# Kernel tuning notes

Hardware: AMD Instinct MI355X
Metric: run time of the kernel (lower is better)

The kernel has to match this reference:

```python
import jax, jax.numpy as jnp
import numpy as np

H = 64  # hidden dim
D_IN = 15  # per-step feature dim


def _gru_layer(x, Wih, Whh, bih, bhh):
    """torch-style GRU, batch_first. x: [M, T, D] -> [M, T, H]."""
    xp = x @ Wih.T + bih  # [M, T, 3H], precomputed input projections

    def step(h, xt):
        gh = h @ Whh.T + bhh
        xr, xz, xn = jnp.split(xt, 3, axis=-1)
        hr, hz, hn = jnp.split(gh, 3, axis=-1)
        r = jax.nn.sigmoid(xr + hr)
        z = jax.nn.sigmoid(xz + hz)
        n = jnp.tanh(xn + r * hn)
        h_new = (1.0 - z) * n + z * h
        return h_new, h_new

    h0 = jnp.zeros((x.shape[0], Whh.shape[1]), x.dtype)
    _, hs = jax.lax.scan(step, h0, jnp.swapaxes(xp, 0, 1))  # [T, M, H]
    return jnp.swapaxes(hs, 0, 1)


def setup_inputs() -> dict:
    key = jax.random.key(0)
    ks = jax.random.split(key, 16)
    N, B, T = 500, 32, 32
    s = 0.05
    return {
        "raw": jax.random.normal(ks[0], (N, B, T, D_IN), dtype=jnp.float32),
        # GRU layer 1 (input 15 -> 64)
        "gru1_Wih": jax.random.normal(ks[1], (3 * H, D_IN), dtype=jnp.float32) * s,
        "gru1_Whh": jax.random.normal(ks[2], (3 * H, H), dtype=jnp.float32) * s,
        "gru1_bih": jax.random.normal(ks[3], (3 * H,), dtype=jnp.float32) * s,
        "gru1_bhh": jax.random.normal(ks[4], (3 * H,), dtype=jnp.float32) * s,
        # GRU layer 2 (64 -> 64)
        "gru2_Wih": jax.random.normal(ks[5], (3 * H, H), dtype=jnp.float32) * s,
        "gru2_Whh": jax.random.normal(ks[6], (3 * H, H), dtype=jnp.float32) * s,
        "gru2_bih": jax.random.normal(ks[7], (3 * H,), dtype=jnp.float32) * s,
        "gru2_bhh": jax.random.normal(ks[8], (3 * H,), dtype=jnp.float32) * s,
        # temporal attention fc (64 -> 1)
        "attn_W": jax.random.normal(ks[9], (1, H), dtype=jnp.float32) * s,
        "attn_b": jax.random.normal(ks[10], (1,), dtype=jnp.float32) * s,
        # GAT attention-block linear W (64 -> 64) and u (128,)
        "gat_W_w": jax.random.normal(ks[11], (H, H), dtype=jnp.float32) * s,
        "gat_W_b": jax.random.normal(ks[12], (H,), dtype=jnp.float32) * s,
        "gat_u": jax.random.normal(ks[13], (2 * H,), dtype=jnp.float32) * s,
        # GAT value projection W1 (64 -> 64)
        "gat_W1_w": jax.random.normal(ks[14], (H, H), dtype=jnp.float32) * s,
        "gat_W1_b": jax.random.normal(ks[15], (H,), dtype=jnp.float32) * s,
    }


def reference(raw, gru1_Wih, gru1_Whh, gru1_bih, gru1_bhh,
              gru2_Wih, gru2_Whh, gru2_bih, gru2_bhh,
              attn_W, attn_b, gat_W_w, gat_W_b, gat_u, gat_W1_w, gat_W1_b):
    N, B, T, D = raw.shape
    x = raw.reshape(N * B, T, D)

    # SequenceEncoder: two stacked GRUs + temporal attention (dropout = eval identity)
    h = _gru_layer(x, gru1_Wih, gru1_Whh, gru1_bih, gru1_bhh)
    h = _gru_layer(h, gru2_Wih, gru2_Whh, gru2_bih, gru2_bhh)  # [NB, T, H]
    scores = jnp.tanh(h @ attn_W.T + attn_b)                    # [NB, T, 1]
    w = jax.nn.softmax(scores, axis=1)                          # softmax over time
    Ai = jnp.sum(h * w, axis=1).reshape(N, B, H)                # [N, B, H]

    # GAT over all-to-all node graph
    sq = Ai @ gat_W_w.T + gat_W_b          # attention-block projection [N, B, H]
    s_q = sq @ gat_u[:H]                   # query-side score [N, B]
    s_k = sq @ gat_u[H:]                   # neighbor-side score [N, B]
    score = s_q[:, None, :] + s_k[None, :, :]                   # [Nq, Nk, B]
    beta = jnp.exp(jax.nn.leaky_relu(score, negative_slope=0.01))
    beta = beta / jnp.sum(beta, axis=1, keepdims=True)          # normalize over neighbors
    proj = Ai @ gat_W1_w.T + gat_W1_b                           # value projection [N, B, H]
    g = jax.nn.relu(jnp.einsum('qkb,kbd->qbd', beta, proj))     # [N, B, H]
    return g
```

## Files before the change

kernel.cpp:

```cpp
#include <hip/hip_runtime.h>

#define TT 32
#define DIN 15
#define LOG2E 1.44269504088896340736f

typedef _Float16 f16x8 __attribute__((ext_vector_type(8)));
typedef _Float16 f16x4 __attribute__((ext_vector_type(4)));
typedef float f32x4 __attribute__((ext_vector_type(4)));

__device__ __forceinline__ float rcp_(float x){ return __builtin_amdgcn_rcpf(x); }
__device__ __forceinline__ float exp2_(float x){ return __builtin_amdgcn_exp2f(x); }
__device__ __forceinline__ float tanh_(float x){ return fmaf(-2.f, rcp_(__expf(2.f*x)+1.f), 1.f); }

#define MFMA(a,b,c) __builtin_amdgcn_mfma_f32_16x16x32_f16(a,b,c,0,0,0)

__device__ __forceinline__ f16x8 f16x8_zero(){
  f16x8 v;
  #pragma unroll
  for (int j=0;j<8;++j) v[j]=(_Float16)0.f;
  return v;
}

__global__ void wprep(const float* __restrict__ w1ih, const float* __restrict__ w1hh,
                      const float* __restrict__ w2ih, const float* __restrict__ w2hh,
                      const float* __restrict__ b1ih, const float* __restrict__ b1hh,
                      const float* __restrict__ W1,
                      const float* __restrict__ Ww, const float* __restrict__ Wb,
                      const float* __restrict__ u,
                      _Float16* __restrict__ wf, float* __restrict__ vqk){
  int id = blockIdx.x*256 + threadIdx.x;
  if (id < 47104){
    int e = id & 7, c = id >> 3;
    float v, scale;
    if (c < 4608){
      int mat = c / 1536; int r = c - mat*1536;
      int lane = r & 63, kf = (r>>6)&1, q = r>>7;
      const float* W = (mat==0)? w1hh : (mat==1)? w2ih : w2hh;
      int ht = q/3, g3 = q - ht*3;
      int row = g3*64 + ht*16 + (lane & 15);
      int k = kf*32 + (lane>>4)*8 + e;
      v = W[row*64 + k];
      scale = (g3==2) ? 2.f*LOG2E : -LOG2E;
    } else if (c < 5376){
      int r = c - 4608; int lane = r & 63, q = r>>6;
      int ht = q/3, g3 = q - ht*3;
      int row = g3*64 + ht*16 + (lane & 15);
      int k = (lane>>4)*8 + e;
      if (k < DIN)       v = w1ih[row*DIN + k];
      else if (k == DIN) v = (g3 < 2) ? (b1ih[row] + b1hh[row]) : b1ih[row];
      else               v = 0.f;
      scale = (g3==2) ? 2.f*LOG2E : -LOG2E;
    } else {
      int r = c - 5376; int lane = r & 63, q = r>>6;
      int ht = q>>1, kf = q&1;
      int row = ht*16 + (lane & 15);
      int k = kf*32 + (lane>>4)*8 + e;
      v = W1[row*64 + k]; scale = 1.f;
    }
    wf[c*8 + e] = (_Float16)(v*scale);
  } else if (id < 47104 + 130){
    int t = id - 47104;
    if (t < 128){
      int which = t>>6, j = t&63;
      float s = 0.f;
      for (int i=0;i<64;++i) s = fmaf(u[which*64+i], Ww[i*64+j], s);
      vqk[t] = s;
    } else {
      int which = t-128;
      float s = 0.f;
      for (int i=0;i<64;++i) s = fmaf(u[which*64+i], Wb[i], s);
      vqk[128+which] = s;
    }
  }
}

__global__ __launch_bounds__(256, 2) void gru_mfma(
    const float* __restrict__ raw,
    const _Float16* __restrict__ wf,
    const float* __restrict__ vqk,
    const float* __restrict__ bhh1,
    const float* __restrict__ bih2, const float* __restrict__ bhh2,
    const float* __restrict__ attnW, const float* __restrict__ attnb,
    const float* __restrict__ W1b,
    _Float16* __restrict__ projh, float* __restrict__ sqT, float* __restrict__ skT)
{
  __shared__ _Float16 xfh[TT*64*8];
  __shared__ _Float16 h1s[2][32*64];
  __shared__ _Float16 h2s[2][32*64];
  __shared__ float bias2[256];
  __shared__ float attp[2][2][4][16];
  __shared__ float attq[4][32], attk[4][32];

  const int tid  = threadIdx.x;
  const int lane = tid & 63;
  const int ht   = tid >> 6;
  const int g    = lane >> 4;
  const int sl   = lane & 15;
  const int s7   = sl & 7;
  const int n    = blockIdx.x;
  const int seq0 = n*32;
  const int row0 = ht*16 + g*4;

  { int* z2 = (int*)h2s[0]; for (int i=tid; i<1024; i+=256) z2[i]=0; }
  if (tid < 64){
    bias2[tid]       = -(bih2[tid]      + bhh2[tid])   *LOG2E;
    bias2[64+tid]    = -(bih2[64+tid]   + bhh2[64+tid])*LOG2E;
    bias2[128+tid]   =  bih2[128+tid]*(2.f*LOG2E);
    bias2[192+tid]   =  bhh2[128+tid]*(2.f*LOG2E);
  }
  for (int idx=tid; idx<TT*32; idx+=256){
    int s = idx & 31, t = idx >> 5;
    const float* rp = &raw[(size_t)(seq0+s)*(TT*DIN) + t*DIN];
    f16x8 lo, hi;
    #pragma unroll
    for (int j=0;j<8;++j){
      lo[j] = (_Float16)rp[j];
      hi[j] = (j<7) ? (_Float16)rp[8+j] : (_Float16)1.0f;
    }
    *(f16x8*)(xfh + ((size_t)t*64 +      s)*8) = lo;
    *(f16x8*)(xfh + ((size_t)t*64 + 32 + s)*8) = hi;
  }

  const f16x8* wf8 = (const f16x8*)wf;
  f16x8 wr1_0 = wf8[((ht*3+0)*2+0)*64 + lane], wr1_1 = wf8[((ht*3+0)*2+1)*64 + lane];
  f16x8 wz1_0 = wf8[((ht*3+1)*2+0)*64 + lane], wz1_1 = wf8[((ht*3+1)*2+1)*64 + lane];
  f16x8 wn1_0 = wf8[((ht*3+2)*2+0)*64 + lane], wn1_1 = wf8[((ht*3+2)*2+1)*64 + lane];
  f16x8 ar2_0 = wf8[1536+((ht*3+0)*2+0)*64 + lane], ar2_1 = wf8[1536+((ht*3+0)*2+1)*64 + lane];
  f16x8 az2_0 = wf8[1536+((ht*3+1)*2+0)*64 + lane], az2_1 = wf8[1536+((ht*3+1)*2+1)*64 + lane];
  f16x8 an2_0 = wf8[1536+((ht*3+2)*2+0)*64 + lane], an2_1 = wf8[1536+((ht*3+2)*2+1)*64 + lane];
  f16x8 br2_0 = wf8[3072+((ht*3+0)*2+0)*64 + lane], br2_1 = wf8[3072+((ht*3+0)*2+1)*64 + lane];
  f16x8 bz2_0 = wf8[3072+((ht*3+1)*2+0)*64 + lane], bz2_1 = wf8[3072+((ht*3+1)*2+1)*64 + lane];
  f16x8 bn2_0 = wf8[3072+((ht*3+2)*2+0)*64 + lane], bn2_1 = wf8[3072+((ht*3+2)*2+1)*64 + lane];
  f16x8 xr1 = wf8[4608 + (ht*3+0)*64 + lane];
  f16x8 xz1 = wf8[4608 + (ht*3+1)*64 + lane];
  f16x8 xn1 = wf8[4608 + (ht*3+2)*64 + lane];

  f32x4 Bhn1, awv;
  #pragma unroll
  for (int r=0;r<4;++r){ Bhn1[r] = bhh1[128+row0+r]*(2.f*LOG2E); awv[r] = attnW[row0+r]; }
  const float ab = attnb[0];

  __syncthreads();

  const f16x8 fz = f16x8_zero();
  f32x4 h1c0={0,0,0,0}, h1c1={0,0,0,0}, h2c0={0,0,0,0}, h2c1={0,0,0,0};
  f32x4 num0={0,0,0,0}, num1={0,0,0,0};
  float den0=0.f, den1=0.f;
  const int cwr = (((ht*2+(g>>1)) ^ s7))*8 + (g&1)*4;

  {
    f16x8 xf0 = fz, xf1 = fz;
    if (g < 2){
      xf0 = *(const f16x8*)(xfh + ((size_t)0*64 + g*32 +      sl)*8);
      xf1 = *(const f16x8*)(xfh + ((size_t)0*64 + g*32 + 16 + sl)*8);
    }
    f32x4 Cr0={0,0,0,0}, Cz0={0,0,0,0}, Cxn0={0,0,0,0}, Chn0=Bhn1;
    f32x4 Cr1={0,0,0,0}, Cz1={0,0,0,0}, Cxn1={0,0,0,0}, Chn1=Bhn1;
    Cr0 = MFMA(xr1,xf0,Cr0); Cz0 = MFMA(xz1,xf0,Cz0); Cxn0 = MFMA(xn1,xf0,Cxn0);
    Cr1 = MFMA(xr1,xf1,Cr1); Cz1 = MFMA(xz1,xf1,Cz1); Cxn1 = MFMA(xn1,xf1,Cxn1);
    f16x4 hw0, hw1;
    #pragma unroll
    for (int r=0;r<4;++r){
      float rg0 = rcp_(1.f + exp2_(Cr0[r]));
      float zg0 = rcp_(1.f + exp2_(Cz0[r]));
      float ng0 = fmaf(-2.f, rcp_(exp2_(Cxn0[r] + rg0*Chn0[r]) + 1.f), 1.f);
      float h0  = ng0 - zg0*ng0;
      h1c0[r] = h0; hw0[r] = (_Float16)h0;
      float rg1 = rcp_(1.f + exp2_(Cr1[r]));
      float zg1 = rcp_(1.f + exp2_(Cz1[r]));
      float ng1 = fmaf(-2.f, rcp_(exp2_(Cxn1[r] + rg1*Chn1[r]) + 1.f), 1.f);
      float h1v = ng1 - zg1*ng1;
      h1c1[r] = h1v; hw1[r] = (_Float16)h1v;
    }
    *(f16x4*)(h1s[0] + sl*64      + cwr) = hw0;
    *(f16x4*)(h1s[0] + (16+sl)*64 + cwr) = hw1;
  }
  __syncthreads();

  #pragma unroll 1
  for (int i=0; i<TT; ++i){
    const _Float16* h1rd = h1s[i&1];
    const _Float16* h2rd = h2s[i&1];
    _Float16* h1wr = h1s[(i+1)&1];
    _Float16* h2wr = h2s[(i+1)&1];
    f16x8 h1f0_0 = *(const f16x8*)(h1rd + sl*64      + ((g    ^s7))*8);
    f16x8 h1f0_1 = *(const f16x8*)(h1rd + sl*64      + (((4+g)^s7))*8);
    f16x8 h1f1_0 = *(const f16x8*)(h1rd + (16+sl)*64 + ((g    ^s7))*8);
    f16x8 h1f1_1 = *(const f16x8*)(h1rd + (16+sl)*64 + (((4+g)^s7))*8);
    f16x8 h2f0_0 = *(const f16x8*)(h2rd + sl*64      + ((g    ^s7))*8);
    f16x8 h2f0_1 = *(const f16x8*)(h2rd + sl*64      + (((4+g)^s7))*8);
    f16x8 h2f1_0 = *(const f16x8*)(h2rd + (16+sl)*64 + ((g    ^s7))*8);
    f16x8 h2f1_1 = *(const f16x8*)(h2rd + (16+sl)*64 + (((4+g)^s7))*8);
    const int tn = (i < TT-1) ? i+1 : TT-1;
    f16x8 xf0 = fz, xf1 = fz;
    if (g < 2){
      xf0 = *(const f16x8*)(xfh + ((size_t)tn*64 + g*32 +      sl)*8);
      xf1 = *(const f16x8*)(xfh + ((size_t)tn*64 + g*32 + 16 + sl)*8);
    }
    if (i > 0){
      const float (*ap)[4][16] = attp[(i+1)&1];
      float s40 = ap[0][0][sl]+ap[0][1][sl]+ap[0][2][sl]+ap[0][3][sl];
      float s41 = ap[1][0][sl]+ap[1][1][sl]+ap[1][2][sl]+ap[1][3][sl];
      float e0 = __expf(tanh_(s40 + ab));
      float e1 = __expf(tanh_(s41 + ab));
      den0 += e0; den1 += e1;
      #pragma unroll
      for (int r=0;r<4;++r){
        num0[r] = fmaf(e0, h2c0[r], num0[r]);
        num1[r] = fmaf(e1, h2c1[r], num1[r]);
      }
    }
    f32x4 Dr0  = *(const f32x4*)(bias2 + row0);
    f32x4 Dz0  = *(const f32x4*)(bias2 + 64 + row0);
    f32x4 Dxn0 = *(const f32x4*)(bias2 + 128 + row0);
    f32x4 Dhn0 = *(const f32x4*)(bias2 + 192 + row0);
    f32x4 Dr1 = Dr0, Dz1 = Dz0, Dxn1 = Dxn0, Dhn1 = Dhn0;
    Dr0  = MFMA(ar2_0,h1f0_0,Dr0);  Dr0  = MFMA(ar2_1,h1f0_1,Dr0);
    Dr0  = MFMA(br2_0,h2f0_0,Dr0);  Dr0  = MFMA(br2_1,h2f0_1,Dr0);
    Dr1  = MFMA(ar2_0,h1f1_0,Dr1);  Dr1  = MFMA(ar2_1,h1f1_1,Dr1);
    Dr1  = MFMA(br2_0,h2f1_0,Dr1);  Dr1  = MFMA(br2_1,h2f1_1,Dr1);
    Dz0  = MFMA(az2_0,h1f0_0,Dz0);  Dz0  = MFMA(az2_1,h1f0_1,Dz0);
    Dz0  = MFMA(bz2_0,h2f0_0,Dz0);  Dz0  = MFMA(bz2_1,h2f0_1,Dz0);
    Dz1  = MFMA(az2_0,h1f1_0,Dz1);  Dz1  = MFMA(az2_1,h1f1_1,Dz1);
    Dz1  = MFMA(bz2_0,h2f1_0,Dz1);  Dz1  = MFMA(bz2_1,h2f1_1,Dz1);
    Dxn0 = MFMA(an2_0,h1f0_0,Dxn0); Dxn0 = MFMA(an2_1,h1f0_1,Dxn0);
    Dxn1 = MFMA(an2_0,h1f1_0,Dxn1); Dxn1 = MFMA(an2_1,h1f1_1,Dxn1);
    Dhn0 = MFMA(bn2_0,h2f0_0,Dhn0); Dhn0 = MFMA(bn2_1,h2f0_1,Dhn0);
    Dhn1 = MFMA(bn2_0,h2f1_0,Dhn1); Dhn1 = MFMA(bn2_1,h2f1_1,Dhn1);
    f32x4 Cr0={0,0,0,0}, Cz0={0,0,0,0}, Cxn0={0,0,0,0}, Chn0=Bhn1;
    f32x4 Cr1={0,0,0,0}, Cz1={0,0,0,0}, Cxn1={0,0,0,0}, Chn1=Bhn1;
    Cr0 = MFMA(wr1_0,h1f0_0,Cr0); Cr0 = MFMA(wr1_1,h1f0_1,Cr0); Cr0 = MFMA(xr1,xf0,Cr0);
    Cr1 = MFMA(wr1_0,h1f1_0,Cr1); Cr1 = MFMA(wr1_1,h1f1_1,Cr1); Cr1 = MFMA(xr1,xf1,Cr1);
    Cz0 = MFMA(wz1_0,h1f0_0,Cz0); Cz0 = MFMA(wz1_1,h1f0_1,Cz0); Cz0 = MFMA(xz1,xf0,Cz0);
    Cz1 = MFMA(wz1_0,h1f1_0,Cz1); Cz1 = MFMA(wz1_1,h1f1_1,Cz1); Cz1 = MFMA(xz1,xf1,Cz1);
    Chn0 = MFMA(wn1_0,h1f0_0,Chn0); Chn0 = MFMA(wn1_1,h1f0_1,Chn0);
    Chn1 = MFMA(wn1_0,h1f1_0,Chn1); Chn1 = MFMA(wn1_1,h1f1_1,Chn1);
    Cxn0 = MFMA(xn1,xf0,Cxn0);
    Cxn1 = MFMA(xn1,xf1,Cxn1);
    f16x4 hw0, hw1;
    float p0 = 0.f, p1 = 0.f;
    #pragma unroll
    for (int r=0;r<4;++r){
      float rg0 = rcp_(1.f + exp2_(Dr0[r]));
      float zg0 = rcp_(1.f + exp2_(Dz0[r]));
      float ng0 = fmaf(-2.f, rcp_(exp2_(Dxn0[r] + rg0*Dhn0[r]) + 1.f), 1.f);
      float h0  = ng0 + zg0*(h2c0[r] - ng0);
      h2c0[r] = h0; hw0[r] = (_Float16)h0;
      p0 = fmaf(h0, awv[r], p0);
      float rg1 = rcp_(1.f + exp2_(Dr1[r]));
      float zg1 = rcp_(1.f + exp2_(Dz1[r]));
      float ng1 = fmaf(-2.f, rcp_(exp2_(Dxn1[r] + rg1*Dhn1[r]) + 1.f), 1.f);
      float h1v = ng1 + zg1*(h2c1[r] - ng1);
      h2c1[r] = h1v; hw1[r] = (_Float16)h1v;
      p1 = fmaf(h1v, awv[r], p1);
    }
    *(f16x4*)(h2wr + sl*64      + cwr) = hw0;
    *(f16x4*)(h2wr + (16+sl)*64 + cwr) = hw1;
    p0 += __shfl_xor(p0, 16, 64); p0 += __shfl_xor(p0, 32, 64);
    p1 += __shfl_xor(p1, 16, 64); p1 += __shfl_xor(p1, 32, 64);
    if (lane < 16){ attp[i&1][0][ht][sl] = p0; attp[i&1][1][ht][sl] = p1; }
    if (i < TT-1){
      #pragma unroll
      for (int r=0;r<4;++r){
        float rg0 = rcp_(1.f + exp2_(Cr0[r]));
        float zg0 = rcp_(1.f + exp2_(Cz0[r]));
        float ng0 = fmaf(-2.f, rcp_(exp2_(Cxn0[r] + rg0*Chn0[r]) + 1.f), 1.f);
        float h0  = ng0 + zg0*(h1c0[r] - ng0);
        h1c0[r] = h0; hw0[r] = (_Float16)h0;
        float rg1 = rcp_(1.f + exp2_(Cr1[r]));
        float zg1 = rcp_(1.f + exp2_(Cz1[r]));
        float ng1 = fmaf(-2.f, rcp_(exp2_(Cxn1[r] + rg1*Chn1[r]) + 1.f), 1.f);
        float h1v = ng1 + zg1*(h1c1[r] - ng1);
        h1c1[r] = h1v; hw1[r] = (_Float16)h1v;
      }
      *(f16x4*)(h1wr + sl*64      + cwr) = hw0;
      *(f16x4*)(h1wr + (16+sl)*64 + cwr) = hw1;
    }
    __syncthreads();
  }
  {
    const float (*ap)[4][16] = attp[1];
    float s40 = ap[0][0][sl]+ap[0][1][sl]+ap[0][2][sl]+ap[0][3][sl];
    float s41 = ap[1][0][sl]+ap[1][1][sl]+ap[1][2][sl]+ap[1][3][sl];
    float e0 = __expf(tanh_(s40 + ab));
    float e1 = __expf(tanh_(s41 + ab));
    den0 += e0; den1 += e1;
    #pragma unroll
    for (int r=0;r<4;++r){
      num0[r] = fmaf(e0, h2c0[r], num0[r]);
      num1[r] = fmaf(e1, h2c1[r], num1[r]);
    }
  }
  float rd0 = rcp_(den0), rd1 = rcp_(den1);
  f32x4 av0, av1;
  #pragma unroll
  for (int r=0;r<4;++r){ av0[r] = num0[r]*rd0; av1[r] = num1[r]*rd1; }
  {
    f32x4 vq4 = *(const f32x4*)&vqk[row0];
    f32x4 vk4 = *(const f32x4*)&vqk[64+row0];
    float pq0=0.f, pk0=0.f, pq1=0.f, pk1=0.f;
    #pragma unroll
    for (int r=0;r<4;++r){
      pq0 = fmaf(av0[r], vq4[r], pq0); pk0 = fmaf(av0[r], vk4[r], pk0);
      pq1 = fmaf(av1[r], vq4[r], pq1); pk1 = fmaf(av1[r], vk4[r], pk1);
    }
    pq0 += __shfl_xor(pq0,16,64); pq0 += __shfl_xor(pq0,32,64);
    pk0 += __shfl_xor(pk0,16,64); pk0 += __shfl_xor(pk0,32,64);
    pq1 += __shfl_xor(pq1,16,64); pq1 += __shfl_xor(pq1,32,64);
    pk1 += __shfl_xor(pk1,16,64); pk1 += __shfl_xor(pk1,32,64);
    if (lane < 16){
      attq[ht][sl] = pq0;    attk[ht][sl] = pk0;
      attq[ht][16+sl] = pq1; attk[ht][16+sl] = pk1;
    }
  }
  { f16x4 af0, af1;
    #pragma unroll
    for (int r=0;r<4;++r){ af0[r] = (_Float16)av0[r]; af1[r] = (_Float16)av1[r]; }
    *(f16x4*)(h1s[0] + sl*64      + cwr) = af0;
    *(f16x4*)(h1s[0] + (16+sl)*64 + cwr) = af1; }
  __syncthreads();
  if (tid < 32){
    float q4 = attq[0][tid]+attq[1][tid]+attq[2][tid]+attq[3][tid];
    float k4 = attk[0][tid]+attk[1][tid]+attk[2][tid]+attk[3][tid];
    sqT[tid*512 + n] = (q4 + vqk[128])*LOG2E;
    skT[tid*512 + n] = (k4 + vqk[129])*LOG2E;
  }
  {
    f16x8 a0 = wf8[5376 + (ht*2+0)*64 + lane];
    f16x8 a1 = wf8[5376 + (ht*2+1)*64 + lane];
    f16x8 b00 = *(const f16x8*)(h1s[0] + sl*64      + ((g    ^s7))*8);
    f16x8 b01 = *(const f16x8*)(h1s[0] + sl*64      + (((4+g)^s7))*8);
    f16x8 b10 = *(const f16x8*)(h1s[0] + (16+sl)*64 + ((g    ^s7))*8);
    f16x8 b11 = *(const f16x8*)(h1s[0] + (16+sl)*64 + (((4+g)^s7))*8);
    f32x4 P0 = *(const f32x4*)&W1b[row0];
    f32x4 P1 = P0;
    P0 = MFMA(a0,b00,P0); P0 = MFMA(a1,b01,P0);
    P1 = MFMA(a0,b10,P1); P1 = MFMA(a1,b11,P1);
    f16x4 pf0, pf1;
    #pragma unroll
    for (int r=0;r<4;++r){ pf0[r] = (_Float16)P0[r]; pf1[r] = (_Float16)P1[r]; }
    *(f16x4*)(projh + (size_t)(seq0+sl)*64    + row0) = pf0;
    *(f16x4*)(projh + (size_t)(seq0+16+sl)*64 + row0) = pf1;
  }
}

__global__ __launch_bounds__(256) void gat_agg(
    const _Float16* __restrict__ projh,
    const float* __restrict__ sqT, const float* __restrict__ skT,
    float* __restrict__ out)
{
  __shared__ _Float16 pT[64*64];
  __shared__ float sks[512];
  const int tid  = threadIdx.x;
  const int lane = tid & 63;
  const int wv   = tid >> 6;
  const int b    = blockIdx.x & 31;
  const int qt   = blockIdx.x >> 5;
  const int sl   = lane & 15, g = lane >> 4;
  const int myq  = qt*64 + wv*16 + sl;
  const float sq_l = (myq < 500) ? sqT[b*512 + myq] : -1e30f;
  for (int j = tid; j < 512; j += 256) sks[j] = (j < 500) ? skT[b*512 + j] : -1e30f;

  f32x4 acc[4] = {{0,0,0,0},{0,0,0,0},{0,0,0,0},{0,0,0,0}};
  float den_l = 0.f;
  const int kr = tid & 63, dgrp = tid >> 6;

  f16x8 pv0 = f16x8_zero(), pv1 = f16x8_zero();
  if (kr < 500){
    const f16x8* pp = (const f16x8*)(projh + ((size_t)kr*32 + b)*64 + dgrp*16);
    pv0 = pp[0]; pv1 = pp[1];
  }

  #pragma unroll 1
  for (int kc=0; kc<8; ++kc){
    __syncthreads();
    { char* base = (char*)pT;
      const int klo = (kr & 7) << 1, khi = kr >> 3;
      #pragma unroll
      for (int j=0;j<16;++j){
        int d = dgrp*16 + j;
        _Float16 v = (j<8) ? pv0[j] : pv1[j-8];
        *(_Float16*)(base + d*128 + (((khi ^ (d&7))) << 4) + klo) = v;
      } }
    __syncthreads();
    if (kc < 7){
      int node = (kc+1)*64 + kr;
      if (node < 500){
        const f16x8* pp = (const f16x8*)(projh + ((size_t)node*32 + b)*64 + dgrp*16);
        pv0 = pp[0]; pv1 = pp[1];
      } else { pv0 = f16x8_zero(); pv1 = f16x8_zero(); }
    }
    #pragma unroll
    for (int kc32=0; kc32<2; ++kc32){
      const int kb = kc*64 + kc32*32 + g*8;
      float4 skv0 = *(const float4*)&sks[kb];
      float4 skv1 = *(const float4*)&sks[kb+4];
      float s[8] = {sq_l+skv0.x, sq_l+skv0.y, sq_l+skv0.z, sq_l+skv0.w,
                    sq_l+skv1.x, sq_l+skv1.y, sq_l+skv1.z, sq_l+skv1.w};
      f16x8 bf;
      #pragma unroll
      for (int e=0;e<8;++e){
        float sc = fmaxf(s[e], 0.01f*s[e]);
        float ev = exp2_(sc);
        den_l += ev;
        bf[e] = (_Float16)ev;
      }
      const char* base = (const char*)pT;
      #pragma unroll
      for (int dt=0; dt<4; ++dt){
        f16x8 a = *(const f16x8*)(base + (dt*16 + sl)*128 + (((kc32*4 + g) ^ (sl&7)) << 4));
        acc[dt] = MFMA(a, bf, acc[dt]);
      }
    }
  }
  den_l += __shfl_xor(den_l, 16, 64);
  den_l += __shfl_xor(den_l, 32, 64);
  const float rd = rcp_(den_l);
  if (myq < 500){
    #pragma unroll
    for (int dt=0; dt<4; ++dt){
      f32x4 o;
      #pragma unroll
      for (int r=0;r<4;++r) o[r] = fmaxf(acc[dt][r]*rd, 0.f);
      *(f32x4*)&out[((size_t)myq*32 + b)*64 + dt*16 + g*4] = o;
    }
  }
}

extern "C" void kernel_launch(void* const* d_in, const int* in_sizes, int n_in,
                              void* d_out, int out_size, void* d_ws, size_t ws_size,
                              hipStream_t stream) {
  const float* raw   = (const float*)d_in[0];
  const float* w1ih  = (const float*)d_in[1];
  const float* w1hh  = (const float*)d_in[2];
  const float* b1ih  = (const float*)d_in[3];
  const float* b1hh  = (const float*)d_in[4];
  const float* w2ih  = (const float*)d_in[5];
  const float* w2hh  = (const float*)d_in[6];
  const float* b2ih  = (const float*)d_in[7];
  const float* b2hh  = (const float*)d_in[8];
  const float* attW  = (const float*)d_in[9];
  const float* attb  = (const float*)d_in[10];
  const float* gWw   = (const float*)d_in[11];
  const float* gWb   = (const float*)d_in[12];
  const float* gu    = (const float*)d_in[13];
  const float* gW1   = (const float*)d_in[14];
  const float* gW1b  = (const float*)d_in[15];
  float* outp = (float*)d_out;

  char* wsb = (char*)d_ws;
  _Float16* projh = (_Float16*)wsb;
  float*    sqT   = (float*)(wsb + 2048000);
  float*    skT   = (float*)(wsb + 2048000 + 65536);
  _Float16* wfh   = (_Float16*)(wsb + 2048000 + 131072);
  float*    vqk   = (float*)(wsb + 2048000 + 131072 + 94208);

  wprep<<<185, 256, 0, stream>>>(w1ih, w1hh, w2ih, w2hh, b1ih, b1hh,
                                 gW1, gWw, gWb, gu, wfh, vqk);
  gru_mfma<<<500, 256, 0, stream>>>(raw, wfh, vqk, b1hh, b2ih, b2hh,
                                    attW, attb, gW1b, projh, sqT, skT);
  gat_agg<<<256, 256, 0, stream>>>(projh, sqT, skT, outp);
}
```

Before: 92.24 us.

## Split GRU layers across warp roles in a 512-thread block

The block doubles to 512 threads. Waves 0-3 run the layer-1 GRU recurrence and waves 4-7 run layer-2 plus the temporal attention, so the two layers advance in a wavefront within each time step. Each wave now keeps only one layer's weights in registers. The aim is to halve the serial MFMA and transcendental chain per wave per step and to relieve register pressure. In exchange it adds more waves per block that must synchronise at every step, and the layer-2 state is reread from LDS as fp16 rather than kept in fp32 registers.

```diff
diff --git a/kernel.cpp b/kernel.cpp
--- a/kernel.cpp
+++ b/kernel.cpp
@@ -74,7 +74,7 @@
   }
 }
 
-__global__ __launch_bounds__(256, 2) void gru_mfma(
+__global__ __launch_bounds__(512, 4) void gru_mfma(
     const float* __restrict__ raw,
     const _Float16* __restrict__ wf,
     const float* __restrict__ vqk,
@@ -93,22 +93,27 @@
 
   const int tid  = threadIdx.x;
   const int lane = tid & 63;
-  const int ht   = tid >> 6;
+  const int wid  = tid >> 6;
+  const int role = wid >> 2;
+  const int ht   = wid & 3;
   const int g    = lane >> 4;
   const int sl   = lane & 15;
   const int s7   = sl & 7;
   const int n    = blockIdx.x;
   const int seq0 = n*32;
   const int row0 = ht*16 + g*4;
-
-  { int* z2 = (int*)h2s[0]; for (int i=tid; i<1024; i+=256) z2[i]=0; }
+  const int cwr  = (((ht*2+(g>>1)) ^ s7))*8 + (g&1)*4;
+  const int oT0  = sl*64, oT1 = (16+sl)*64;
+  const int c0   = (g ^ s7)*8, c1 = ((4+g) ^ s7)*8;
+
+  { int* z2 = (int*)h2s[0]; for (int i=tid; i<1024; i+=512) z2[i]=0; }
   if (tid < 64){
     bias2[tid]       = -(bih2[tid]      + bhh2[tid])   *LOG2E;
     bias2[64+tid]    = -(bih2[64+tid]   + bhh2[64+tid])*LOG2E;
     bias2[128+tid]   =  bih2[128+tid]*(2.f*LOG2E);
     bias2[192+tid]   =  bhh2[128+tid]*(2.f*LOG2E);
   }
-  for (int idx=tid; idx<TT*32; idx+=256){
+  for (int idx=tid; idx<TT*32; idx+=512){
     int s = idx & 31, t = idx >> 5;
     const float* rp = &raw[(size_t)(seq0+s)*(TT*DIN) + t*DIN];
     f16x8 lo, hi;
@@ -122,180 +127,195 @@
   }
 
   const f16x8* wf8 = (const f16x8*)wf;
-  f16x8 wr1_0 = wf8[((ht*3+0)*2+0)*64 + lane], wr1_1 = wf8[((ht*3+0)*2+1)*64 + lane];
-  f16x8 wz1_0 = wf8[((ht*3+1)*2+0)*64 + lane], wz1_1 = wf8[((ht*3+1)*2+1)*64 + lane];
-  f16x8 wn1_0 = wf8[((ht*3+2)*2+0)*64 + lane], wn1_1 = wf8[((ht*3+2)*2+1)*64 + lane];
-  f16x8 ar2_0 = wf8[1536+((ht*3+0)*2+0)*64 + lane], ar2_1 = wf8[1536+((ht*3+0)*2+1)*64 + lane];
-  f16x8 az2_0 = wf8[1536+((ht*3+1)*2+0)*64 + lane], az2_1 = wf8[1536+((ht*3+1)*2+1)*64 + lane];
-  f16x8 an2_0 = wf8[1536+((ht*3+2)*2+0)*64 + lane], an2_1 = wf8[1536+((ht*3+2)*2+1)*64 + lane];
-  f16x8 br2_0 = wf8[3072+((ht*3+0)*2+0)*64 + lane], br2_1 = wf8[3072+((ht*3+0)*2+1)*64 + lane];
-  f16x8 bz2_0 = wf8[3072+((ht*3+1)*2+0)*64 + lane], bz2_1 = wf8[3072+((ht*3+1)*2+1)*64 + lane];
-  f16x8 bn2_0 = wf8[3072+((ht*3+2)*2+0)*64 + lane], bn2_1 = wf8[3072+((ht*3+2)*2+1)*64 + lane];
-  f16x8 xr1 = wf8[4608 + (ht*3+0)*64 + lane];
-  f16x8 xz1 = wf8[4608 + (ht*3+1)*64 + lane];
-  f16x8 xn1 = wf8[4608 + (ht*3+2)*64 + lane];
-
-  f32x4 Bhn1, awv;
-  #pragma unroll
-  for (int r=0;r<4;++r){ Bhn1[r] = bhh1[128+row0+r]*(2.f*LOG2E); awv[r] = attnW[row0+r]; }
+  const f16x8 fz = f16x8_zero();
+  f16x8 A0,A1,A2,A3,A4,A5,A6,A7,A8,A9,A10,A11;
+  f32x4 BC;
   const float ab = attnb[0];
+  if (role == 0){
+    A0 = wf8[((ht*3+0)*2+0)*64 + lane]; A1 = wf8[((ht*3+0)*2+1)*64 + lane];
+    A2 = wf8[((ht*3+1)*2+0)*64 + lane]; A3 = wf8[((ht*3+1)*2+1)*64 + lane];
+    A4 = wf8[((ht*3+2)*2+0)*64 + lane]; A5 = wf8[((ht*3+2)*2+1)*64 + lane];
+    A6 = wf8[4608 + (ht*3+0)*64 + lane];
+    A7 = wf8[4608 + (ht*3+1)*64 + lane];
+    A8 = wf8[4608 + (ht*3+2)*64 + lane];
+    A9  = wf8[5376 + (ht*2+0)*64 + lane];
+    A10 = wf8[5376 + (ht*2+1)*64 + lane];
+    A11 = fz;
+    #pragma unroll
+    for (int r=0;r<4;++r) BC[r] = bhh1[128+row0+r]*(2.f*LOG2E);
+  } else {
+    A0 = wf8[1536+((ht*3+0)*2+0)*64+lane]; A1 = wf8[1536+((ht*3+0)*2+1)*64+lane];
+    A2 = wf8[1536+((ht*3+1)*2+0)*64+lane]; A3 = wf8[1536+((ht*3+1)*2+1)*64+lane];
+    A4 = wf8[1536+((ht*3+2)*2+0)*64+lane]; A5 = wf8[1536+((ht*3+2)*2+1)*64+lane];
+    A6 = wf8[3072+((ht*3+0)*2+0)*64+lane]; A7 = wf8[3072+((ht*3+0)*2+1)*64+lane];
+    A8 = wf8[3072+((ht*3+1)*2+0)*64+lane]; A9 = wf8[3072+((ht*3+1)*2+1)*64+lane];
+    A10= wf8[3072+((ht*3+2)*2+0)*64+lane]; A11= wf8[3072+((ht*3+2)*2+1)*64+lane];
+    #pragma unroll
+    for (int r=0;r<4;++r) BC[r] = attnW[row0+r];
+  }
+
+  f32x4 S0 = {0,0,0,0}, S1 = {0,0,0,0};
+  float d0 = 0.f, d1 = 0.f;
 
   __syncthreads();
 
-  const f16x8 fz = f16x8_zero();
-  f32x4 h1c0={0,0,0,0}, h1c1={0,0,0,0}, h2c0={0,0,0,0}, h2c1={0,0,0,0};
-  f32x4 num0={0,0,0,0}, num1={0,0,0,0};
-  float den0=0.f, den1=0.f;
-  const int cwr = (((ht*2+(g>>1)) ^ s7))*8 + (g&1)*4;
-
-  {
+  if (role == 0){
     f16x8 xf0 = fz, xf1 = fz;
     if (g < 2){
       xf0 = *(const f16x8*)(xfh + ((size_t)0*64 + g*32 +      sl)*8);
       xf1 = *(const f16x8*)(xfh + ((size_t)0*64 + g*32 + 16 + sl)*8);
     }
-    f32x4 Cr0={0,0,0,0}, Cz0={0,0,0,0}, Cxn0={0,0,0,0}, Chn0=Bhn1;
-    f32x4 Cr1={0,0,0,0}, Cz1={0,0,0,0}, Cxn1={0,0,0,0}, Chn1=Bhn1;
-    Cr0 = MFMA(xr1,xf0,Cr0); Cz0 = MFMA(xz1,xf0,Cz0); Cxn0 = MFMA(xn1,xf0,Cxn0);
-    Cr1 = MFMA(xr1,xf1,Cr1); Cz1 = MFMA(xz1,xf1,Cz1); Cxn1 = MFMA(xn1,xf1,Cxn1);
+    f32x4 Cr0={0,0,0,0}, Cz0={0,0,0,0}, Cxn0={0,0,0,0};
+    f32x4 Cr1={0,0,0,0}, Cz1={0,0,0,0}, Cxn1={0,0,0,0};
+    Cr0 = MFMA(A6,xf0,Cr0); Cz0 = MFMA(A7,xf0,Cz0); Cxn0 = MFMA(A8,xf0,Cxn0);
+    Cr1 = MFMA(A6,xf1,Cr1); Cz1 = MFMA(A7,xf1,Cz1); Cxn1 = MFMA(A8,xf1,Cxn1);
     f16x4 hw0, hw1;
     #pragma unroll
     for (int r=0;r<4;++r){
       float rg0 = rcp_(1.f + exp2_(Cr0[r]));
       float zg0 = rcp_(1.f + exp2_(Cz0[r]));
-      float ng0 = fmaf(-2.f, rcp_(exp2_(Cxn0[r] + rg0*Chn0[r]) + 1.f), 1.f);
+      float ng0 = fmaf(-2.f, rcp_(exp2_(Cxn0[r] + rg0*BC[r]) + 1.f), 1.f);
       float h0  = ng0 - zg0*ng0;
-      h1c0[r] = h0; hw0[r] = (_Float16)h0;
+      S0[r] = h0; hw0[r] = (_Float16)h0;
       float rg1 = rcp_(1.f + exp2_(Cr1[r]));
       float zg1 = rcp_(1.f + exp2_(Cz1[r]));
-      float ng1 = fmaf(-2.f, rcp_(exp2_(Cxn1[r] + rg1*Chn1[r]) + 1.f), 1.f);
+      float ng1 = fmaf(-2.f, rcp_(exp2_(Cxn1[r] + rg1*BC[r]) + 1.f), 1.f);
       float h1v = ng1 - zg1*ng1;
-      h1c1[r] = h1v; hw1[r] = (_Float16)h1v;
-    }
-    *(f16x4*)(h1s[0] + sl*64      + cwr) = hw0;
-    *(f16x4*)(h1s[0] + (16+sl)*64 + cwr) = hw1;
+      S1[r] = h1v; hw1[r] = (_Float16)h1v;
+    }
+    *(f16x4*)(h1s[0] + oT0 + cwr) = hw0;
+    *(f16x4*)(h1s[0] + oT1 + cwr) = hw1;
   }
   __syncthreads();
 
   #pragma unroll 1
   for (int i=0; i<TT; ++i){
-    const _Float16* h1rd = h1s[i&1];
-    const _Float16* h2rd = h2s[i&1];
-    _Float16* h1wr = h1s[(i+1)&1];
-    _Float16* h2wr = h2s[(i+1)&1];
-    f16x8 h1f0_0 = *(const f16x8*)(h1rd + sl*64      + ((g    ^s7))*8);
-    f16x8 h1f0_1 = *(const f16x8*)(h1rd + sl*64      + (((4+g)^s7))*8);
-    f16x8 h1f1_0 = *(const f16x8*)(h1rd + (16+sl)*64 + ((g    ^s7))*8);
-    f16x8 h1f1_1 = *(const f16x8*)(h1rd + (16+sl)*64 + (((4+g)^s7))*8);
-    f16x8 h2f0_0 = *(const f16x8*)(h2rd + sl*64      + ((g    ^s7))*8);
-    f16x8 h2f0_1 = *(const f16x8*)(h2rd + sl*64      + (((4+g)^s7))*8);
-    f16x8 h2f1_0 = *(const f16x8*)(h2rd + (16+sl)*64 + ((g    ^s7))*8);
-    f16x8 h2f1_1 = *(const f16x8*)(h2rd + (16+sl)*64 + (((4+g)^s7))*8);
-    const int tn = (i < TT-1) ? i+1 : TT-1;
-    f16x8 xf0 = fz, xf1 = fz;
-    if (g < 2){
-      xf0 = *(const f16x8*)(xfh + ((size_t)tn*64 + g*32 +      sl)*8);
-      xf1 = *(const f16x8*)(xfh + ((size_t)tn*64 + g*32 + 16 + sl)*8);
-    }
-    if (i > 0){
-      const float (*ap)[4][16] = attp[(i+1)&1];
+    if (role == 0){
+      if (i < TT-1){
+        const _Float16* h1rd = h1s[i&1];
+        _Float16* h1wr = h1s[(i+1)&1];
+        f16x8 xf0 = fz, xf1 = fz;
+        if (g < 2){
+          xf0 = *(const f16x8*)(xfh + ((size_t)(i+1)*64 + g*32 +      sl)*8);
+          xf1 = *(const f16x8*)(xfh + ((size_t)(i+1)*64 + g*32 + 16 + sl)*8);
+        }
+        f32x4 Cr0={0,0,0,0}, Cz0={0,0,0,0}, Cxn0={0,0,0,0}, Chn0=BC;
+        f32x4 Cr1={0,0,0,0}, Cz1={0,0,0,0}, Cxn1={0,0,0,0}, Chn1=BC;
+        f16x8 f0 = *(const f16x8*)(h1rd + oT0 + c0);
+        f16x8 f1 = *(const f16x8*)(h1rd + oT1 + c0);
+        Cr0 = MFMA(A0,f0,Cr0); Cz0 = MFMA(A2,f0,Cz0); Chn0 = MFMA(A4,f0,Chn0);
+        Cr1 = MFMA(A0,f1,Cr1); Cz1 = MFMA(A2,f1,Cz1); Chn1 = MFMA(A4,f1,Chn1);
+        Cr0 = MFMA(A6,xf0,Cr0); Cz0 = MFMA(A7,xf0,Cz0); Cxn0 = MFMA(A8,xf0,Cxn0);
+        Cr1 = MFMA(A6,xf1,Cr1); Cz1 = MFMA(A7,xf1,Cz1); Cxn1 = MFMA(A8,xf1,Cxn1);
+        f0 = *(const f16x8*)(h1rd + oT0 + c1);
+        f1 = *(const f16x8*)(h1rd + oT1 + c1);
+        Cr0 = MFMA(A1,f0,Cr0); Cz0 = MFMA(A3,f0,Cz0); Chn0 = MFMA(A5,f0,Chn0);
+        Cr1 = MFMA(A1,f1,Cr1); Cz1 = MFMA(A3,f1,Cz1); Chn1 = MFMA(A5,f1,Chn1);
+        f16x4 hw0, hw1;
+        #pragma unroll
+        for (int r=0;r<4;++r){
+          float rg0 = rcp_(1.f + exp2_(Cr0[r]));
+          float zg0 = rcp_(1.f + exp2_(Cz0[r]));
+          float ng0 = fmaf(-2.f, rcp_(exp2_(Cxn0[r] + rg0*Chn0[r]) + 1.f), 1.f);
+          float h0  = ng0 + zg0*(S0[r] - ng0);
+          S0[r] = h0; hw0[r] = (_Float16)h0;
+          float rg1 = rcp_(1.f + exp2_(Cr1[r]));
+          float zg1 = rcp_(1.f + exp2_(Cz1[r]));
+          float ng1 = fmaf(-2.f, rcp_(exp2_(Cxn1[r] + rg1*Chn1[r]) + 1.f), 1.f);
+          float h1v = ng1 + zg1*(S1[r] - ng1);
+          S1[r] = h1v; hw1[r] = (_Float16)h1v;
+        }
+        *(f16x4*)(h1wr + oT0 + cwr) = hw0;
+        *(f16x4*)(h1wr + oT1 + cwr) = hw1;
+      }
+    } else {
+      const _Float16* h1rd = h1s[i&1];
+      const _Float16* h2rd = h2s[i&1];
+      _Float16* h2wr = h2s[(i+1)&1];
+      f16x4 ho0 = *(const f16x4*)(h2rd + oT0 + cwr);
+      f16x4 ho1 = *(const f16x4*)(h2rd + oT1 + cwr);
+      if (i > 0){
+        const float (*ap)[4][16] = attp[(i+1)&1];
+        float s40 = ap[0][0][sl]+ap[0][1][sl]+ap[0][2][sl]+ap[0][3][sl];
+        float s41 = ap[1][0][sl]+ap[1][1][sl]+ap[1][2][sl]+ap[1][3][sl];
+        float e0 = __expf(tanh_(s40 + ab));
+        float e1 = __expf(tanh_(s41 + ab));
+        d0 += e0; d1 += e1;
+        #pragma unroll
+        for (int r=0;r<4;++r){
+          S0[r] = fmaf(e0, (float)ho0[r], S0[r]);
+          S1[r] = fmaf(e1, (float)ho1[r], S1[r]);
+        }
+      }
+      f32x4 Dr0  = *(const f32x4*)(bias2 + row0);
+      f32x4 Dz0  = *(const f32x4*)(bias2 + 64 + row0);
+      f32x4 Dxn0 = *(const f32x4*)(bias2 + 128 + row0);
+      f32x4 Dhn0 = *(const f32x4*)(bias2 + 192 + row0);
+      f32x4 Dr1 = Dr0, Dz1 = Dz0, Dxn1 = Dxn0, Dhn1 = Dhn0;
+      f16x8 f10 = *(const f16x8*)(h1rd + oT0 + c0);
+      f16x8 f11 = *(const f16x8*)(h1rd + oT1 + c0);
+      f16x8 f20 = *(const f16x8*)(h2rd + oT0 + c0);
+      f16x8 f21 = *(const f16x8*)(h2rd + oT1 + c0);
+      Dr0  = MFMA(A0,f10,Dr0);  Dr0  = MFMA(A6,f20,Dr0);
+      Dr1  = MFMA(A0,f11,Dr1);  Dr1  = MFMA(A6,f21,Dr1);
+      Dz0  = MFMA(A2,f10,Dz0);  Dz0  = MFMA(A8,f20,Dz0);
+      Dz1  = MFMA(A2,f11,Dz1);  Dz1  = MFMA(A8,f21,Dz1);
+      Dxn0 = MFMA(A4,f10,Dxn0); Dxn1 = MFMA(A4,f11,Dxn1);
+      Dhn0 = MFMA(A10,f20,Dhn0); Dhn1 = MFMA(A10,f21,Dhn1);
+      f10 = *(const f16x8*)(h1rd + oT0 + c1);
+      f11 = *(const f16x8*)(h1rd + oT1 + c1);
+      f20 = *(const f16x8*)(h2rd + oT0 + c1);
+      f21 = *(const f16x8*)(h2rd + oT1 + c1);
+      Dr0  = MFMA(A1,f10,Dr0);  Dr0  = MFMA(A7,f20,Dr0);
+      Dr1  = MFMA(A1,f11,Dr1);  Dr1  = MFMA(A7,f21,Dr1);
+      Dz0  = MFMA(A3,f10,Dz0);  Dz0  = MFMA(A9,f20,Dz0);
+      Dz1  = MFMA(A3,f11,Dz1);  Dz1  = MFMA(A9,f21,Dz1);
+      Dxn0 = MFMA(A5,f10,Dxn0); Dxn1 = MFMA(A5,f11,Dxn1);
+      Dhn0 = MFMA(A11,f20,Dhn0); Dhn1 = MFMA(A11,f21,Dhn1);
+      f16x4 hw0, hw1;
+      float p0 = 0.f, p1 = 0.f;
+      #pragma unroll
+      for (int r=0;r<4;++r){
+        float rg0 = rcp_(1.f + exp2_(Dr0[r]));
+        float zg0 = rcp_(1.f + exp2_(Dz0[r]));
+        float ng0 = fmaf(-2.f, rcp_(exp2_(Dxn0[r] + rg0*Dhn0[r]) + 1.f), 1.f);
+        float h0  = ng0 + zg0*((float)ho0[r] - ng0);
+        hw0[r] = (_Float16)h0; p0 = fmaf(h0, BC[r], p0);
+        float rg1 = rcp_(1.f + exp2_(Dr1[r]));
+        float zg1 = rcp_(1.f + exp2_(Dz1[r]));
+        float ng1 = fmaf(-2.f, rcp_(exp2_(Dxn1[r] + rg1*Dhn1[r]) + 1.f), 1.f);
+        float h1v = ng1 + zg1*((float)ho1[r] - ng1);
+        hw1[r] = (_Float16)h1v; p1 = fmaf(h1v, BC[r], p1);
+      }
+      *(f16x4*)(h2wr + oT0 + cwr) = hw0;
+      *(f16x4*)(h2wr + oT1 + cwr) = hw1;
+      p0 += __shfl_xor(p0, 16, 64); p0 += __shfl_xor(p0, 32, 64);
+      p1 += __shfl_xor(p1, 16, 64); p1 += __shfl_xor(p1, 32, 64);
+      if (lane < 16){ attp[i&1][0][ht][sl] = p0; attp[i&1][1][ht][sl] = p1; }
+    }
+    __syncthreads();
+  }
+
+  if (role == 1){
+    f16x4 ho0 = *(const f16x4*)(h2s[0] + oT0 + cwr);
+    f16x4 ho1 = *(const f16x4*)(h2s[0] + oT1 + cwr);
+    {
+      const float (*ap)[4][16] = attp[1];
       float s40 = ap[0][0][sl]+ap[0][1][sl]+ap[0][2][sl]+ap[0][3][sl];
       float s41 = ap[1][0][sl]+ap[1][1][sl]+ap[1][2][sl]+ap[1][3][sl];
       float e0 = __expf(tanh_(s40 + ab));
       float e1 = __expf(tanh_(s41 + ab));
-      den0 += e0; den1 += e1;
+      d0 += e0; d1 += e1;
       #pragma unroll
       for (int r=0;r<4;++r){
-        num0[r] = fmaf(e0, h2c0[r], num0[r]);
-        num1[r] = fmaf(e1, h2c1[r], num1[r]);
-      }
-    }
-    f32x4 Dr0  = *(const f32x4*)(bias2 + row0);
-    f32x4 Dz0  = *(const f32x4*)(bias2 + 64 + row0);
-    f32x4 Dxn0 = *(const f32x4*)(bias2 + 128 + row0);
-    f32x4 Dhn0 = *(const f32x4*)(bias2 + 192 + row0);
-    f32x4 Dr1 = Dr0, Dz1 = Dz0, Dxn1 = Dxn0, Dhn1 = Dhn0;
-    Dr0  = MFMA(ar2_0,h1f0_0,Dr0);  Dr0  = MFMA(ar2_1,h1f0_1,Dr0);
-    Dr0  = MFMA(br2_0,h2f0_0,Dr0);  Dr0  = MFMA(br2_1,h2f0_1,Dr0);
-    Dr1  = MFMA(ar2_0,h1f1_0,Dr1);  Dr1  = MFMA(ar2_1,h1f1_1,Dr1);
-    Dr1  = MFMA(br2_0,h2f1_0,Dr1);  Dr1  = MFMA(br2_1,h2f1_1,Dr1);
-    Dz0  = MFMA(az2_0,h1f0_0,Dz0);  Dz0  = MFMA(az2_1,h1f0_1,Dz0);
-    Dz0  = MFMA(bz2_0,h2f0_0,Dz0);  Dz0  = MFMA(bz2_1,h2f0_1,Dz0);
-    Dz1  = MFMA(az2_0,h1f1_0,Dz1);  Dz1  = MFMA(az2_1,h1f1_1,Dz1);
-    Dz1  = MFMA(bz2_0,h2f1_0,Dz1);  Dz1  = MFMA(bz2_1,h2f1_1,Dz1);
-    Dxn0 = MFMA(an2_0,h1f0_0,Dxn0); Dxn0 = MFMA(an2_1,h1f0_1,Dxn0);
-    Dxn1 = MFMA(an2_0,h1f1_0,Dxn1); Dxn1 = MFMA(an2_1,h1f1_1,Dxn1);
-    Dhn0 = MFMA(bn2_0,h2f0_0,Dhn0); Dhn0 = MFMA(bn2_1,h2f0_1,Dhn0);
-    Dhn1 = MFMA(bn2_0,h2f1_0,Dhn1); Dhn1 = MFMA(bn2_1,h2f1_1,Dhn1);
-    f32x4 Cr0={0,0,0,0}, Cz0={0,0,0,0}, Cxn0={0,0,0,0}, Chn0=Bhn1;
-    f32x4 Cr1={0,0,0,0}, Cz1={0,0,0,0}, Cxn1={0,0,0,0}, Chn1=Bhn1;
-    Cr0 = MFMA(wr1_0,h1f0_0,Cr0); Cr0 = MFMA(wr1_1,h1f0_1,Cr0); Cr0 = MFMA(xr1,xf0,Cr0);
-    Cr1 = MFMA(wr1_0,h1f1_0,Cr1); Cr1 = MFMA(wr1_1,h1f1_1,Cr1); Cr1 = MFMA(xr1,xf1,Cr1);
-    Cz0 = MFMA(wz1_0,h1f0_0,Cz0); Cz0 = MFMA(wz1_1,h1f0_1,Cz0); Cz0 = MFMA(xz1,xf0,Cz0);
-    Cz1 = MFMA(wz1_0,h1f1_0,Cz1); Cz1 = MFMA(wz1_1,h1f1_1,Cz1); Cz1 = MFMA(xz1,xf1,Cz1);
-    Chn0 = MFMA(wn1_0,h1f0_0,Chn0); Chn0 = MFMA(wn1_1,h1f0_1,Chn0);
-    Chn1 = MFMA(wn1_0,h1f1_0,Chn1); Chn1 = MFMA(wn1_1,h1f1_1,Chn1);
-    Cxn0 = MFMA(xn1,xf0,Cxn0);
-    Cxn1 = MFMA(xn1,xf1,Cxn1);
-    f16x4 hw0, hw1;
-    float p0 = 0.f, p1 = 0.f;
-    #pragma unroll
-    for (int r=0;r<4;++r){
-      float rg0 = rcp_(1.f + exp2_(Dr0[r]));
-      float zg0 = rcp_(1.f + exp2_(Dz0[r]));
-      float ng0 = fmaf(-2.f, rcp_(exp2_(Dxn0[r] + rg0*Dhn0[r]) + 1.f), 1.f);
-      float h0  = ng0 + zg0*(h2c0[r] - ng0);
-      h2c0[r] = h0; hw0[r] = (_Float16)h0;
-      p0 = fmaf(h0, awv[r], p0);
-      float rg1 = rcp_(1.f + exp2_(Dr1[r]));
-      float zg1 = rcp_(1.f + exp2_(Dz1[r]));
-      float ng1 = fmaf(-2.f, rcp_(exp2_(Dxn1[r] + rg1*Dhn1[r]) + 1.f), 1.f);
-      float h1v = ng1 + zg1*(h2c1[r] - ng1);
-      h2c1[r] = h1v; hw1[r] = (_Float16)h1v;
-      p1 = fmaf(h1v, awv[r], p1);
-    }
-    *(f16x4*)(h2wr + sl*64      + cwr) = hw0;
-    *(f16x4*)(h2wr + (16+sl)*64 + cwr) = hw1;
-    p0 += __shfl_xor(p0, 16, 64); p0 += __shfl_xor(p0, 32, 64);
-    p1 += __shfl_xor(p1, 16, 64); p1 += __shfl_xor(p1, 32, 64);
-    if (lane < 16){ attp[i&1][0][ht][sl] = p0; attp[i&1][1][ht][sl] = p1; }
-    if (i < TT-1){
-      #pragma unroll
-      for (int r=0;r<4;++r){
-        float rg0 = rcp_(1.f + exp2_(Cr0[r]));
-        float zg0 = rcp_(1.f + exp2_(Cz0[r]));
-        float ng0 = fmaf(-2.f, rcp_(exp2_(Cxn0[r] + rg0*Chn0[r]) + 1.f), 1.f);
-        float h0  = ng0 + zg0*(h1c0[r] - ng0);
-        h1c0[r] = h0; hw0[r] = (_Float16)h0;
-        float rg1 = rcp_(1.f + exp2_(Cr1[r]));
-        float zg1 = rcp_(1.f + exp2_(Cz1[r]));
-        float ng1 = fmaf(-2.f, rcp_(exp2_(Cxn1[r] + rg1*Chn1[r]) + 1.f), 1.f);
-        float h1v = ng1 + zg1*(h1c1[r] - ng1);
-        h1c1[r] = h1v; hw1[r] = (_Float16)h1v;
-      }
-      *(f16x4*)(h1wr + sl*64      + cwr) = hw0;
-      *(f16x4*)(h1wr + (16+sl)*64 + cwr) = hw1;
-    }
-    __syncthreads();
-  }
-  {
-    const float (*ap)[4][16] = attp[1];
-    float s40 = ap[0][0][sl]+ap[0][1][sl]+ap[0][2][sl]+ap[0][3][sl];
-    float s41 = ap[1][0][sl]+ap[1][1][sl]+ap[1][2][sl]+ap[1][3][sl];
-    float e0 = __expf(tanh_(s40 + ab));
-    float e1 = __expf(tanh_(s41 + ab));
-    den0 += e0; den1 += e1;
-    #pragma unroll
-    for (int r=0;r<4;++r){
-      num0[r] = fmaf(e0, h2c0[r], num0[r]);
-      num1[r] = fmaf(e1, h2c1[r], num1[r]);
-    }
-  }
-  float rd0 = rcp_(den0), rd1 = rcp_(den1);
-  f32x4 av0, av1;
-  #pragma unroll
-  for (int r=0;r<4;++r){ av0[r] = num0[r]*rd0; av1[r] = num1[r]*rd1; }
-  {
+        S0[r] = fmaf(e0, (float)ho0[r], S0[r]);
+        S1[r] = fmaf(e1, (float)ho1[r], S1[r]);
+      }
+    }
+    float rd0 = rcp_(d0), rd1 = rcp_(d1);
+    f32x4 av0, av1;
+    #pragma unroll
+    for (int r=0;r<4;++r){ av0[r] = S0[r]*rd0; av1[r] = S1[r]*rd1; }
     f32x4 vq4 = *(const f32x4*)&vqk[row0];
     f32x4 vk4 = *(const f32x4*)&vqk[64+row0];
     float pq0=0.f, pk0=0.f, pq1=0.f, pk1=0.f;
@@ -312,35 +332,34 @@
       attq[ht][sl] = pq0;    attk[ht][sl] = pk0;
       attq[ht][16+sl] = pq1; attk[ht][16+sl] = pk1;
     }
-  }
-  { f16x4 af0, af1;
+    f16x4 af0, af1;
     #pragma unroll
     for (int r=0;r<4;++r){ af0[r] = (_Float16)av0[r]; af1[r] = (_Float16)av1[r]; }
-    *(f16x4*)(h1s[0] + sl*64      + cwr) = af0;
-    *(f16x4*)(h1s[0] + (16+sl)*64 + cwr) = af1; }
+    *(f16x4*)(h1s[0] + oT0 + cwr) = af0;
+    *(f16x4*)(h1s[0] + oT1 + cwr) = af1;
+  }
   __syncthreads();
+
+  if (role == 0){
+    f16x8 b00 = *(const f16x8*)(h1s[0] + oT0 + c0);
+    f16x8 b01 = *(const f16x8*)(h1s[0] + oT0 + c1);
+    f16x8 b10 = *(const f16x8*)(h1s[0] + oT1 + c0);
+    f16x8 b11 = *(const f16x8*)(h1s[0] + oT1 + c1);
+    f32x4 P0 = *(const f32x4*)&W1b[row0];
+    f32x4 P1 = P0;
+    P0 = MFMA(A9,b00,P0); P0 = MFMA(A10,b01,P0);
+    P1 = MFMA(A9,b10,P1); P1 = MFMA(A10,b11,P1);
+    f16x4 pf0, pf1;
+    #pragma unroll
+    for (int r=0;r<4;++r){ pf0[r] = (_Float16)P0[r]; pf1[r] = (_Float16)P1[r]; }
+    *(f16x4*)(projh + (size_t)(seq0+sl)*64    + row0) = pf0;
+    *(f16x4*)(projh + (size_t)(seq0+16+sl)*64 + row0) = pf1;
+  }
   if (tid < 32){
     float q4 = attq[0][tid]+attq[1][tid]+attq[2][tid]+attq[3][tid];
     float k4 = attk[0][tid]+attk[1][tid]+attk[2][tid]+attk[3][tid];
     sqT[tid*512 + n] = (q4 + vqk[128])*LOG2E;
     skT[tid*512 + n] = (k4 + vqk[129])*LOG2E;
-  }
-  {
-    f16x8 a0 = wf8[5376 + (ht*2+0)*64 + lane];
-    f16x8 a1 = wf8[5376 + (ht*2+1)*64 + lane];
-    f16x8 b00 = *(const f16x8*)(h1s[0] + sl*64      + ((g    ^s7))*8);
-    f16x8 b01 = *(const f16x8*)(h1s[0] + sl*64      + (((4+g)^s7))*8);
-    f16x8 b10 = *(const f16x8*)(h1s[0] + (16+sl)*64 + ((g    ^s7))*8);
-    f16x8 b11 = *(const f16x8*)(h1s[0] + (16+sl)*64 + (((4+g)^s7))*8);
-    f32x4 P0 = *(const f32x4*)&W1b[row0];
-    f32x4 P1 = P0;
-    P0 = MFMA(a0,b00,P0); P0 = MFMA(a1,b01,P0);
-    P1 = MFMA(a0,b10,P1); P1 = MFMA(a1,b11,P1);
-    f16x4 pf0, pf1;
-    #pragma unroll
-    for (int r=0;r<4;++r){ pf0[r] = (_Float16)P0[r]; pf1[r] = (_Float16)P1[r]; }
-    *(f16x4*)(projh + (size_t)(seq0+sl)*64    + row0) = pf0;
-    *(f16x4*)(projh + (size_t)(seq0+16+sl)*64 + row0) = pf1;
   }
 }
 
@@ -457,7 +476,7 @@
 
   wprep<<<185, 256, 0, stream>>>(w1ih, w1hh, w2ih, w2hh, b1ih, b1hh,
                                  gW1, gWw, gWb, gu, wfh, vqk);
-  gru_mfma<<<500, 256, 0, stream>>>(raw, wfh, vqk, b1hh, b2ih, b2hh,
+  gru_mfma<<<500, 512, 0, stream>>>(raw, wfh, vqk, b1hh, b2ih, b2hh,
                                     attW, attb, gW1b, projh, sqT, skT);
   gat_agg<<<256, 256, 0, stream>>>(projh, sqT, skT, outp);
 }
```

After: 105.6 us. 14.5% more time.
